# Kernel tuning notes

Hardware: AMD Instinct MI355X
Metric: run time of the kernel (lower is better)

Reference implementation:

```python
import jax, jax.numpy as jnp
import numpy as np

B, D, Q = 64, 1024, 128
V, E, H = 50000, 300, 256   # vocab, embed_dim, prealign hidden
POS_V, POS_D = 56, 12
NER_V, NER_D = 19, 8


def setup_inputs() -> dict:
    key = jax.random.key(0)
    ks = jax.random.split(key, 10)
    word_emb = (jax.random.normal(ks[0], (V, E), jnp.float32) * 0.1).at[0].set(0.0)
    pos_emb = (jax.random.normal(ks[1], (POS_V, POS_D), jnp.float32) * 0.1).at[0].set(0.0)
    ner_emb = (jax.random.normal(ks[2], (NER_V, NER_D), jnp.float32) * 0.1).at[0].set(0.0)
    proj_w = jax.random.normal(ks[3], (E, H), jnp.float32) / np.sqrt(E)
    proj_b = jnp.zeros((H,), jnp.float32)
    return {
        "query_tok": jax.random.randint(ks[4], (B, Q), 0, V),
        "doc_tok": jax.random.randint(ks[5], (B, D), 0, V),
        "doc_pos": jax.random.randint(ks[6], (B, D), 0, POS_V),
        "doc_ner": jax.random.randint(ks[7], (B, D), 0, NER_V),
        "doc_fea": jax.random.normal(ks[8], (B, D, 4), jnp.float32),
        "word_emb": word_emb,
        "proj_w": proj_w,
        "proj_b": proj_b,
        "pos_emb": pos_emb,
        "ner_emb": ner_emb,
    }


def _embed(table, idx):
    # padding_idx=0 semantics: row 0 contributes zeros
    return table[idx] * (idx != 0)[..., None].astype(table.dtype)


def reference(query_tok, doc_tok, doc_pos, doc_ner, doc_fea,
              word_emb, proj_w, proj_b, pos_emb, ner_emb):
    doc_e = _embed(word_emb, doc_tok)      # [B,D,E]
    query_e = _embed(word_emb, query_tok)  # [B,Q,E]

    # Prealign: shared Linear+ReLU proj, then bmm -> softmax -> bmm
    d_proj = jax.nn.relu(doc_e @ proj_w + proj_b)    # [B,D,H]
    q_proj = jax.nn.relu(query_e @ proj_w + proj_b)  # [B,Q,H]
    scores = jnp.einsum('bdh,bqh->bdq', d_proj, q_proj)
    attn = jax.nn.softmax(scores, axis=-1)           # softmax over query dim
    prealign = jnp.einsum('bdq,bqe->bde', attn, query_e)  # [B,D,E]

    doc_out = jnp.concatenate(
        [doc_e, prealign, _embed(ner_emb, doc_ner), _embed(pos_emb, doc_pos), doc_fea],
        axis=-1)  # [B,D,E+E+8+12+4]
    return query_e, doc_out
```

## Files before the change

kernel.cpp:

```cpp
#include <hip/hip_runtime.h>
#include <hip/hip_bf16.h>

typedef unsigned short u16;
typedef __attribute__((ext_vector_type(8))) short bf16x8;
typedef __attribute__((ext_vector_type(4))) float f32x4;

#define MFMA16(a, b, c) __builtin_amdgcn_mfma_f32_16x16x32_bf16((a), (b), (c), 0, 0, 0)

#define NB 64
#define ND 1024
#define NQ 128
#define NE 300
#define NH 256
#define KP 320
#define QETN 304
#define DOC_W 624

static __device__ __forceinline__ u16 f2bf(float f) {
  union { __bf16 h; u16 u; } c; c.h = (__bf16)f; return c.u;
}

static __device__ __forceinline__ bf16x8 pack8(float4 f0, float4 f1) {
  union { bf16x8 v; u16 u[8]; } r;
  r.u[0] = f2bf(f0.x); r.u[1] = f2bf(f0.y); r.u[2] = f2bf(f0.z); r.u[3] = f2bf(f0.w);
  r.u[4] = f2bf(f1.x); r.u[5] = f2bf(f1.y); r.u[6] = f2bf(f1.z); r.u[7] = f2bf(f1.w);
  return r.v;
}

static __device__ __forceinline__ bf16x8 cvt8(const float* p) {
  return pack8(*(const float4*)p, *(const float4*)(p + 4));
}

__global__ void k_aux(const float* __restrict__ w, u16* __restrict__ wt,
                      const int* __restrict__ qtok, const float* __restrict__ table,
                      float* __restrict__ q_out,
                      const int* __restrict__ ner, const int* __restrict__ pos,
                      const float* __restrict__ fea,
                      const float* __restrict__ ner_emb, const float* __restrict__ pos_emb,
                      float* __restrict__ doc_out) {
  int bx = blockIdx.x;
  if (bx < 320) {
    int idx = bx * 256 + threadIdx.x;
    int n = idx / KP, k = idx % KP;
    wt[idx] = (k < NE) ? f2bf(w[k * NH + n]) : (u16)0;
  } else if (bx < 2720) {
    int idx = (bx - 320) * 256 + threadIdx.x;
    int row = idx / 75, j = idx % 75;
    int k = j * 4;
    float4 v = {0.f, 0.f, 0.f, 0.f};
    int t = qtok[row];
    if (t != 0) v = *(const float4*)(table + (long)t * NE + k);
    *(float4*)(q_out + (long)row * NE + k) = v;
  } else {
    int idx = (bx - 2720) * 256 + threadIdx.x;
    int row = idx / 6, c0 = (idx % 6) * 4;
    float4 v;
    float* vp = (float*)&v;
#pragma unroll
    for (int u = 0; u < 4; ++u) {
      int c = c0 + u;
      float x;
      if (c < 8)       { int t = ner[row]; x = t ? ner_emb[t * 8 + c] : 0.f; }
      else if (c < 20) { int t = pos[row]; x = t ? pos_emb[t * 12 + (c - 8)] : 0.f; }
      else             { x = fea[(long)row * 4 + (c - 20)]; }
      vp[u] = x;
    }
    *(float4*)(doc_out + (long)row * DOC_W + 600 + c0) = v;
  }
}

__launch_bounds__(256)
__global__ void k_qside(const float* __restrict__ qo, const u16* __restrict__ Wt,
                        const float* __restrict__ bias,
                        u16* __restrict__ qP, u16* __restrict__ qet) {
  __shared__ u16 T[64][314];
  int tid = threadIdx.x;
  if (blockIdx.x < 128) {
    int l = tid & 63, w = tid >> 6;
    int lr = l & 15, lg = l >> 4;
    int bm = blockIdx.x * 64 + (w & 1) * 32;
    int bn = (w >> 1) * 128;
    f32x4 acc[2][8] = {};
    const float* xp0 = qo + (long)(bm + lr) * NE + 8 * lg;
    const float* xp1 = xp0 + 16 * NE;
    const u16* wp = Wt + (long)(bn + lr) * KP + 8 * lg;
#pragma unroll 2
    for (int ks = 0; ks < KP; ks += 32) {
      bf16x8 a0 = cvt8(xp0 + ks);
      bf16x8 a1 = cvt8(xp1 + ks);
#pragma unroll
      for (int nt = 0; nt < 8; ++nt) {
        bf16x8 b0 = *(const bf16x8*)(wp + (long)nt * 16 * KP + ks);
        acc[0][nt] = MFMA16(a0, b0, acc[0][nt]);
        acc[1][nt] = MFMA16(a1, b0, acc[1][nt]);
      }
    }
#pragma unroll
    for (int nt = 0; nt < 8; ++nt) {
      int col = bn + nt * 16 + lr;
      float bv = bias[col];
#pragma unroll
      for (int mt = 0; mt < 2; ++mt)
#pragma unroll
        for (int r = 0; r < 4; ++r) {
          int row = bm + mt * 16 + 4 * lg + r;
          float v = acc[mt][nt][r] + bv;
          v = v > 0.f ? v : 0.f;
          qP[(long)row * NH + col] = f2bf(v);
        }
    }
  } else {
    int bx = blockIdx.x - 128;
    int b = bx >> 1, k0 = (bx & 1) * 64;
    const float* src = qo + ((long)b * NQ + k0) * NE;
    for (int i = tid; i < 64 * 75; i += 256) {
      int row = i / 75, j = (i % 75) * 4;
      float4 f = *(const float4*)(src + (long)row * NE + j);
      T[row][j]     = f2bf(f.x); T[row][j + 1] = f2bf(f.y);
      T[row][j + 2] = f2bf(f.z); T[row][j + 3] = f2bf(f.w);
    }
    __syncthreads();
    u16* dst = qet + (long)b * QETN * NQ + k0;
    for (int i = tid; i < QETN * 16; i += 256) {
      int n = i / 16, kq = (i % 16) * 4;
      u16 v[4] = {0, 0, 0, 0};
      if (n < NE) {
        v[0] = T[kq][n]; v[1] = T[kq + 1][n]; v[2] = T[kq + 2][n]; v[3] = T[kq + 3][n];
      }
      *(uint2*)(dst + (long)n * NQ + kq) = *(const uint2*)v;
    }
  }
}

__launch_bounds__(256, 2)
__global__ void k_fused(const int* __restrict__ dtok, const float* __restrict__ emb,
                        float* doc_out, const u16* __restrict__ Wt,
                        const float* __restrict__ bias,
                        const u16* __restrict__ qP, const u16* __restrict__ qeT) {
  __shared__ __align__(16) u16 dp[128][264];
  u16 (*p_lds)[136] = (u16 (*)[136]) & dp[0][0];
  int b = blockIdx.y, chunk = blockIdx.x;
  int l = threadIdx.x & 63, w = threadIdx.x >> 6;
  int lr = l & 15, lg = l >> 4;
  long blkrow = (long)b * ND + chunk * 128;

  {
    int mrow0 = (w & 1) * 64;
    int ncol0 = (w >> 1) * 128;
    bool wr = (w >> 1) == 0;
    const float* arow[4];
    float* drow[4];
#pragma unroll
    for (int mt = 0; mt < 4; ++mt) {
      long r = blkrow + mrow0 + mt * 16 + lr;
      arow[mt] = emb + (long)dtok[r] * NE;
      drow[mt] = doc_out + r * DOC_W;
    }
    const u16* wp = Wt + (long)(ncol0 + lr) * KP + 8 * lg;
    f32x4 acc[4][8] = {};
    int c0 = 8 * lg;
#pragma unroll 3
    for (int ks = 0; ks < 288; ks += 32) {
      bf16x8 a[4];
#pragma unroll
      for (int mt = 0; mt < 4; ++mt) {
        int col = ks + c0;
        float4 f0 = *(const float4*)(arow[mt] + col);
        float4 f1 = *(const float4*)(arow[mt] + col + 4);
        if (wr) {
          *(float4*)(drow[mt] + col) = f0;
          *(float4*)(drow[mt] + col + 4) = f1;
        }
        a[mt] = pack8(f0, f1);
      }
#pragma unroll
      for (int nt = 0; nt < 8; ++nt) {
        bf16x8 bb = *(const bf16x8*)(wp + nt * 16 * KP + ks);
#pragma unroll
        for (int mt = 0; mt < 4; ++mt) acc[mt][nt] = MFMA16(a[mt], bb, acc[mt][nt]);
      }
    }
    {
      const int ks = 288;
      int col = ks + c0;
      float4 z = {0.f, 0.f, 0.f, 0.f};
      bf16x8 a[4];
#pragma unroll
      for (int mt = 0; mt < 4; ++mt) {
        float4 f0 = (col + 4 <= NE) ? *(const float4*)(arow[mt] + col) : z;
        float4 f1 = (col + 8 <= NE) ? *(const float4*)(arow[mt] + col + 4) : z;
        if (wr) {
          if (col + 4 <= NE) *(float4*)(drow[mt] + col) = f0;
          if (col + 8 <= NE) *(float4*)(drow[mt] + col + 4) = f1;
        }
        a[mt] = pack8(f0, f1);
      }
#pragma unroll
      for (int nt = 0; nt < 8; ++nt) {
        bf16x8 bb = *(const bf16x8*)(wp + nt * 16 * KP + ks);
#pragma unroll
        for (int mt = 0; mt < 4; ++mt) acc[mt][nt] = MFMA16(a[mt], bb, acc[mt][nt]);
      }
    }
#pragma unroll
    for (int nt = 0; nt < 8; ++nt) {
      int col = ncol0 + nt * 16 + lr;
      float bv = bias[col];
#pragma unroll
      for (int mt = 0; mt < 4; ++mt)
#pragma unroll
        for (int r = 0; r < 4; ++r) {
          float v = acc[mt][nt][r] + bv;
          dp[mrow0 + mt * 16 + 4 * lg + r][col] = f2bf(v > 0.f ? v : 0.f);
        }
    }
  }
  __syncthreads();

  f32x4 s[2][8] = {};
  {
    const u16* qpp = qP + ((long)b * NQ + lr) * NH + 8 * lg;
#pragma unroll
    for (int ks = 0; ks < NH; ks += 32) {
      bf16x8 a0 = *(const bf16x8*)&dp[w * 32 + lr][ks + 8 * lg];
      bf16x8 a1 = *(const bf16x8*)&dp[w * 32 + 16 + lr][ks + 8 * lg];
#pragma unroll
      for (int nt = 0; nt < 8; ++nt) {
        bf16x8 bb = *(const bf16x8*)(qpp + (long)nt * 16 * NH + ks);
        s[0][nt] = MFMA16(a0, bb, s[0][nt]);
        s[1][nt] = MFMA16(a1, bb, s[1][nt]);
      }
    }
  }
  __syncthreads();

#pragma unroll
  for (int mt = 0; mt < 2; ++mt) {
    f32x4 mx;
#pragma unroll
    for (int r = 0; r < 4; ++r) {
      float m = s[mt][0][r];
#pragma unroll
      for (int nt = 1; nt < 8; ++nt) m = fmaxf(m, s[mt][nt][r]);
      mx[r] = m;
    }
#pragma unroll
    for (int d = 1; d < 16; d <<= 1)
#pragma unroll
      for (int r = 0; r < 4; ++r) mx[r] = fmaxf(mx[r], __shfl_xor(mx[r], d));
    f32x4 sum = {};
#pragma unroll
    for (int nt = 0; nt < 8; ++nt)
#pragma unroll
      for (int r = 0; r < 4; ++r) {
        float p = __expf(s[mt][nt][r] - mx[r]);
        s[mt][nt][r] = p;
        sum[r] += p;
      }
#pragma unroll
    for (int d = 1; d < 16; d <<= 1)
#pragma unroll
      for (int r = 0; r < 4; ++r) sum[r] += __shfl_xor(sum[r], d);
    f32x4 inv;
#pragma unroll
    for (int r = 0; r < 4; ++r) inv[r] = 1.0f / sum[r];
#pragma unroll
    for (int nt = 0; nt < 8; ++nt)
#pragma unroll
      for (int r = 0; r < 4; ++r)
        p_lds[w * 32 + mt * 16 + 4 * lg + r][nt * 16 + lr] = f2bf(s[mt][nt][r] * inv[r]);
  }

  const u16* qtp = qeT + (long)b * QETN * NQ;
  bf16x8 pa[2][4];
#pragma unroll
  for (int mt = 0; mt < 2; ++mt)
#pragma unroll
    for (int ksi = 0; ksi < 4; ++ksi)
      pa[mt][ksi] = *(const bf16x8*)&p_lds[w * 32 + mt * 16 + lr][ksi * 32 + 8 * lg];
#pragma unroll 2
  for (int nt = 0; nt < 19; ++nt) {
    f32x4 acc0 = {}, acc1 = {};
#pragma unroll
    for (int ksi = 0; ksi < 4; ++ksi) {
      bf16x8 bb = *(const bf16x8*)(qtp + (long)(nt * 16 + lr) * NQ + ksi * 32 + 8 * lg);
      acc0 = MFMA16(pa[0][ksi], bb, acc0);
      acc1 = MFMA16(pa[1][ksi], bb, acc1);
    }
    int col = nt * 16 + lr;
    if (col < NE) {
#pragma unroll
      for (int r = 0; r < 4; ++r) {
        long rl0 = blkrow + w * 32 + 4 * lg + r;
        doc_out[rl0 * DOC_W + 300 + col] = acc0[r];
        doc_out[(rl0 + 16) * DOC_W + 300 + col] = acc1[r];
      }
    }
  }
}

extern "C" void kernel_launch(void* const* d_in, const int* in_sizes, int n_in,
                              void* d_out, int out_size, void* d_ws, size_t ws_size,
                              hipStream_t stream) {
  const int *query_tok = nullptr, *doc_tok = nullptr, *doc_pos = nullptr, *doc_ner = nullptr;
  const float *doc_fea = nullptr, *word_emb = nullptr, *proj_w = nullptr,
              *proj_b = nullptr, *pos_emb = nullptr, *ner_emb = nullptr;
  int n65536 = 0;
  for (int i = 0; i < n_in; ++i) {
    switch (in_sizes[i]) {
      case 15000000: word_emb  = (const float*)d_in[i]; break;
      case 262144:   doc_fea   = (const float*)d_in[i]; break;
      case 76800:    proj_w    = (const float*)d_in[i]; break;
      case 8192:     query_tok = (const int*)d_in[i];   break;
      case 256:      proj_b    = (const float*)d_in[i]; break;
      case 672:      pos_emb   = (const float*)d_in[i]; break;
      case 152:      ner_emb   = (const float*)d_in[i]; break;
      case 65536:
        if (n65536 == 0)      doc_tok = (const int*)d_in[i];
        else if (n65536 == 1) doc_pos = (const int*)d_in[i];
        else                  doc_ner = (const int*)d_in[i];
        ++n65536; break;
      default: break;
    }
  }

  float* out = (float*)d_out;
  float* q_out   = out;
  float* doc_out = out + (size_t)NB * NQ * NE;

  char* ws = (char*)d_ws;
  u16* Wt  = (u16*)ws; ws += (size_t)NH * KP * 2;
  u16* qP  = (u16*)ws; ws += (size_t)NB * NQ * NH * 2;
  u16* qeT = (u16*)ws; ws += (size_t)NB * QETN * NQ * 2;

  k_aux<<<dim3(4256), dim3(256), 0, stream>>>(
      proj_w, Wt, query_tok, word_emb, q_out,
      doc_ner, doc_pos, doc_fea, ner_emb, pos_emb, doc_out);
  k_qside<<<dim3(256), dim3(256), 0, stream>>>(q_out, Wt, proj_b, qP, qeT);
  k_fused<<<dim3(ND / 128, NB), dim3(256), 0, stream>>>(
      doc_tok, word_emb, doc_out, Wt, proj_b, qP, qeT);
}
```

Before: 129.9 us.

## Give each wave full-width projection rows and software-prefetch embedding loads

```diff
diff --git a/kernel.cpp b/kernel.cpp
--- a/kernel.cpp
+++ b/kernel.cpp
@@ -143,79 +143,71 @@
   int l = threadIdx.x & 63, w = threadIdx.x >> 6;
   int lr = l & 15, lg = l >> 4;
   long blkrow = (long)b * ND + chunk * 128;
+  int c0 = 8 * lg;
 
   {
-    int mrow0 = (w & 1) * 64;
-    int ncol0 = (w >> 1) * 128;
-    bool wr = (w >> 1) == 0;
-    const float* arow[4];
-    float* drow[4];
-#pragma unroll
-    for (int mt = 0; mt < 4; ++mt) {
-      long r = blkrow + mrow0 + mt * 16 + lr;
-      arow[mt] = emb + (long)dtok[r] * NE;
-      drow[mt] = doc_out + r * DOC_W;
-    }
-    const u16* wp = Wt + (long)(ncol0 + lr) * KP + 8 * lg;
-    f32x4 acc[4][8] = {};
-    int c0 = 8 * lg;
-#pragma unroll 3
-    for (int ks = 0; ks < 288; ks += 32) {
-      bf16x8 a[4];
-#pragma unroll
-      for (int mt = 0; mt < 4; ++mt) {
-        int col = ks + c0;
-        float4 f0 = *(const float4*)(arow[mt] + col);
-        float4 f1 = *(const float4*)(arow[mt] + col + 4);
-        if (wr) {
-          *(float4*)(drow[mt] + col) = f0;
-          *(float4*)(drow[mt] + col + 4) = f1;
-        }
-        a[mt] = pack8(f0, f1);
-      }
-#pragma unroll
-      for (int nt = 0; nt < 8; ++nt) {
+    long r0 = blkrow + w * 32 + lr;
+    long r1 = r0 + 16;
+    const float* arow0 = emb + (long)dtok[r0] * NE;
+    const float* arow1 = emb + (long)dtok[r1] * NE;
+    float* drow0 = doc_out + r0 * DOC_W;
+    float* drow1 = doc_out + r1 * DOC_W;
+    const u16* wp = Wt + (long)lr * KP + c0;
+    f32x4 acc[2][16] = {};
+    float4 c00 = *(const float4*)(arow0 + c0), c01 = *(const float4*)(arow0 + c0 + 4);
+    float4 c10 = *(const float4*)(arow1 + c0), c11 = *(const float4*)(arow1 + c0 + 4);
+#pragma unroll 1
+    for (int i = 0; i < 9; ++i) {
+      int ks = 32 * i;
+      int ncol = ks + 32 + c0;
+      float4 n00, n01, n10, n11;
+      if (i < 8) {
+        n00 = *(const float4*)(arow0 + ncol); n01 = *(const float4*)(arow0 + ncol + 4);
+        n10 = *(const float4*)(arow1 + ncol); n11 = *(const float4*)(arow1 + ncol + 4);
+      } else {
+        float4 z = {0.f, 0.f, 0.f, 0.f};
+        n00 = (ncol + 4 <= NE) ? *(const float4*)(arow0 + ncol) : z;
+        n01 = (ncol + 8 <= NE) ? *(const float4*)(arow0 + ncol + 4) : z;
+        n10 = (ncol + 4 <= NE) ? *(const float4*)(arow1 + ncol) : z;
+        n11 = (ncol + 8 <= NE) ? *(const float4*)(arow1 + ncol + 4) : z;
+      }
+      *(float4*)(drow0 + ks + c0) = c00; *(float4*)(drow0 + ks + c0 + 4) = c01;
+      *(float4*)(drow1 + ks + c0) = c10; *(float4*)(drow1 + ks + c0 + 4) = c11;
+      bf16x8 a0 = pack8(c00, c01), a1 = pack8(c10, c11);
+#pragma unroll
+      for (int nt = 0; nt < 16; ++nt) {
         bf16x8 bb = *(const bf16x8*)(wp + nt * 16 * KP + ks);
-#pragma unroll
-        for (int mt = 0; mt < 4; ++mt) acc[mt][nt] = MFMA16(a[mt], bb, acc[mt][nt]);
-      }
+        acc[0][nt] = MFMA16(a0, bb, acc[0][nt]);
+        acc[1][nt] = MFMA16(a1, bb, acc[1][nt]);
+      }
+      c00 = n00; c01 = n01; c10 = n10; c11 = n11;
     }
     {
       const int ks = 288;
       int col = ks + c0;
-      float4 z = {0.f, 0.f, 0.f, 0.f};
-      bf16x8 a[4];
-#pragma unroll
-      for (int mt = 0; mt < 4; ++mt) {
-        float4 f0 = (col + 4 <= NE) ? *(const float4*)(arow[mt] + col) : z;
-        float4 f1 = (col + 8 <= NE) ? *(const float4*)(arow[mt] + col + 4) : z;
-        if (wr) {
-          if (col + 4 <= NE) *(float4*)(drow[mt] + col) = f0;
-          if (col + 8 <= NE) *(float4*)(drow[mt] + col + 4) = f1;
-        }
-        a[mt] = pack8(f0, f1);
-      }
-#pragma unroll
-      for (int nt = 0; nt < 8; ++nt) {
+      if (col + 4 <= NE) { *(float4*)(drow0 + col) = c00; *(float4*)(drow1 + col) = c10; }
+      if (col + 8 <= NE) { *(float4*)(drow0 + col + 4) = c01; *(float4*)(drow1 + col + 4) = c11; }
+      bf16x8 a0 = pack8(c00, c01), a1 = pack8(c10, c11);
+#pragma unroll
+      for (int nt = 0; nt < 16; ++nt) {
         bf16x8 bb = *(const bf16x8*)(wp + nt * 16 * KP + ks);
-#pragma unroll
-        for (int mt = 0; mt < 4; ++mt) acc[mt][nt] = MFMA16(a[mt], bb, acc[mt][nt]);
-      }
-    }
-#pragma unroll
-    for (int nt = 0; nt < 8; ++nt) {
-      int col = ncol0 + nt * 16 + lr;
+        acc[0][nt] = MFMA16(a0, bb, acc[0][nt]);
+        acc[1][nt] = MFMA16(a1, bb, acc[1][nt]);
+      }
+    }
+#pragma unroll
+    for (int nt = 0; nt < 16; ++nt) {
+      int col = nt * 16 + lr;
       float bv = bias[col];
 #pragma unroll
-      for (int mt = 0; mt < 4; ++mt)
-#pragma unroll
-        for (int r = 0; r < 4; ++r) {
-          float v = acc[mt][nt][r] + bv;
-          dp[mrow0 + mt * 16 + 4 * lg + r][col] = f2bf(v > 0.f ? v : 0.f);
-        }
-    }
-  }
-  __syncthreads();
+      for (int r = 0; r < 4; ++r) {
+        float v0 = acc[0][nt][r] + bv;
+        float v1 = acc[1][nt][r] + bv;
+        dp[w * 32 + 4 * lg + r][col] = f2bf(v0 > 0.f ? v0 : 0.f);
+        dp[w * 32 + 16 + 4 * lg + r][col] = f2bf(v1 > 0.f ? v1 : 0.f);
+      }
+    }
+  }
 
   f32x4 s[2][8] = {};
   {
```

Result: slower. 135.4 us (+4.2%).
